# Performance work log

Hardware: AMD Instinct MI355X
Metric: run time of the kernel (lower is better)

The kernel has to match this reference:

```python
import jax, jax.numpy as jnp
import numpy as np
from jax import lax

B, N, HC = 16, 4096, 64
EPS = 1e-5


def _fps(xyz, npoint):
    # xyz: [B,N,3] -> indices [B,npoint]; deterministic start at index 0
    b, n, _ = xyz.shape
    def step(carry, _):
        dist, far = carry
        centroid = jnp.take_along_axis(xyz, far[:, None, None], axis=1)  # [B,1,3]
        d = jnp.sum((xyz - centroid) ** 2, -1)                           # [B,N]
        dist = jnp.minimum(dist, d)
        nxt = jnp.argmax(dist, -1).astype(jnp.int32)
        return (dist, nxt), far
    init = (jnp.full((b, n), 1e10, xyz.dtype), jnp.zeros((b,), jnp.int32))
    _, idx = lax.scan(step, init, None, length=npoint)
    return idx.T


def _index_points(pts, idx):
    # pts [B,N,C], idx [B,...] int -> [B,...,C]
    b = idx.shape[0]
    flat = jnp.take_along_axis(pts, idx.reshape(b, -1)[..., None], axis=1)
    return flat.reshape(idx.shape + (pts.shape[-1],))


def _ball_query(radius, nsample, xyz, new_xyz):
    # torch square_distance: ||a||^2 + ||b||^2 - 2 a.b
    n = xyz.shape[1]
    sqr = (jnp.sum(new_xyz ** 2, -1)[:, :, None] + jnp.sum(xyz ** 2, -1)[:, None, :]
           - 2.0 * jnp.einsum('bsd,bnd->bsn', new_xyz, xyz))          # [B,S,N]
    gi = jnp.where(sqr > radius ** 2, n, jnp.arange(n, dtype=jnp.int32))
    gi = jnp.sort(gi, axis=-1)[:, :, :nsample]
    first = gi[:, :, :1]
    return jnp.where(gi == n, first, gi)


def _mlp_maxpool(x, params):
    # x: [B,S,K,C]; 1x1 conv == per-point matmul; BN in training mode (batch stats)
    for (w, bb, g, be) in params:
        x = jnp.einsum('bskc,cd->bskd', x, w) + bb
        m = jnp.mean(x, axis=(0, 1, 2))
        v = jnp.var(x, axis=(0, 1, 2))
        x = g * (x - m) * lax.rsqrt(v + EPS) + be
        x = jax.nn.relu(x)
    return jnp.max(x, axis=2)  # [B,S,Cout]


def _sa(xyz, points, npoint, radius, nsample, params, group_all):
    # xyz [B,3,N], points [B,D,N] (channel-first, like torch)
    xyzt = jnp.transpose(xyz, (0, 2, 1))
    ptst = jnp.transpose(points, (0, 2, 1))
    if group_all:
        new_xyz = jnp.zeros((xyzt.shape[0], 1, 3), xyzt.dtype)
        new_pts = jnp.concatenate([xyzt[:, None], ptst[:, None]], -1)  # [B,1,N,3+D]
    else:
        fidx = _fps(xyzt, npoint)
        new_xyz = _index_points(xyzt, fidx)                            # [B,S,3]
        gi = _ball_query(radius, nsample, xyzt, new_xyz)               # [B,S,K]
        gxyz = _index_points(xyzt, gi) - new_xyz[:, :, None]           # [B,S,K,3]
        new_pts = jnp.concatenate([gxyz, _index_points(ptst, gi)], -1)
    feat = _mlp_maxpool(new_pts, params)                               # [B,S,Cout]
    return jnp.transpose(new_xyz, (0, 2, 1)), jnp.transpose(feat, (0, 2, 1))


def setup_inputs() -> dict:
    key = jax.random.key(0)
    ks = jax.random.split(key, 8)
    inp = {
        'l0_xyz': jax.random.normal(ks[0], (B, 3, N), jnp.float32),
        'l0_points': jax.random.normal(ks[1], (B, 3, N), jnp.float32),
    }
    dims = {'sa1': [(6, HC), (HC, HC * 2)],
            'sa2': [(HC * 2 + 3, HC * 2), (HC * 2, HC * 4)],
            'sa3': [(HC * 4 + 3, HC * 4), (HC * 4, HC * 8)]}
    i = 2
    for name, layers in dims.items():
        for j, (cin, cout) in enumerate(layers, 1):
            inp[f'{name}_w{j}'] = jax.random.normal(ks[i], (cin, cout), jnp.float32) * (1.0 / np.sqrt(cin))
            inp[f'{name}_b{j}'] = jnp.zeros((cout,), jnp.float32)
            inp[f'{name}_g{j}'] = jnp.ones((cout,), jnp.float32)
            inp[f'{name}_be{j}'] = jnp.zeros((cout,), jnp.float32)
            i += 1
    return inp


def reference(l0_xyz, l0_points,
              sa1_w1, sa1_b1, sa1_g1, sa1_be1, sa1_w2, sa1_b2, sa1_g2, sa1_be2,
              sa2_w1, sa2_b1, sa2_g1, sa2_be1, sa2_w2, sa2_b2, sa2_g2, sa2_be2,
              sa3_w1, sa3_b1, sa3_g1, sa3_be1, sa3_w2, sa3_b2, sa3_g2, sa3_be2):
    p1 = [(sa1_w1, sa1_b1, sa1_g1, sa1_be1), (sa1_w2, sa1_b2, sa1_g2, sa1_be2)]
    p2 = [(sa2_w1, sa2_b1, sa2_g1, sa2_be1), (sa2_w2, sa2_b2, sa2_g2, sa2_be2)]
    p3 = [(sa3_w1, sa3_b1, sa3_g1, sa3_be1), (sa3_w2, sa3_b2, sa3_g2, sa3_be2)]
    l1_xyz, l1_points = _sa(l0_xyz, l0_points, 256, 0.2, 32, p1, False)
    l2_xyz, l2_points = _sa(l1_xyz, l1_points, 128, 0.25, 64, p2, False)
    l3_xyz, l3_points = _sa(l2_xyz, l2_points, None, None, None, p3, True)
    x = l3_points.reshape(-1, HC * 8)
    return (l1_xyz, l1_points, l2_xyz, l2_points, l3_xyz, x)
```

## Files before the change

### kernel.cpp

```cpp
#include <hip/hip_runtime.h>
#include <cstddef>


#define EPSB 1e-5f
constexpr int SLOTS1 = 16;
constexpr int SLOTS2 = 64;

static __device__ __forceinline__ unsigned long long umax64(unsigned long long a,
                                                            unsigned long long b)
{
    return a > b ? a : b;
}

static __device__ __forceinline__ unsigned pack_bf16x2(float a, float b)
{
    unsigned ua = __float_as_uint(a), ub = __float_as_uint(b);
    ua += 0x7fffu + ((ua >> 16) & 1u);
    ub += 0x7fffu + ((ub >> 16) & 1u);
    return (ua >> 16) | (ub & 0xffff0000u);
}

static __device__ __forceinline__ unsigned short bf16_of(float a)
{
    unsigned u = __float_as_uint(a);
    u += 0x7fffu + ((u >> 16) & 1u);
    return (unsigned short)(u >> 16);
}

static __device__ __forceinline__ unsigned long long wave_umax64_dpp(unsigned long long x)
{
#define DPP_STEP(ctrl, rmask)                                                        \
    {                                                                                \
        int lo_ = __builtin_amdgcn_update_dpp(0, (int)(unsigned)x, ctrl, rmask, 0xf, false); \
        int hi_ = __builtin_amdgcn_update_dpp(0, (int)(unsigned)(x >> 32), ctrl, rmask, 0xf, false); \
        unsigned long long c_ = ((unsigned long long)(unsigned)hi_ << 32) | (unsigned)lo_; \
        x = umax64(x, c_);                                                           \
    }
    DPP_STEP(0x111, 0xf)
    DPP_STEP(0x112, 0xf)
    DPP_STEP(0x114, 0xf)
    DPP_STEP(0x118, 0xf)
    DPP_STEP(0x142, 0xa)
    DPP_STEP(0x143, 0xc)
#undef DPP_STEP
    unsigned lo = (unsigned)__builtin_amdgcn_readlane((int)(unsigned)x, 63);
    unsigned hi = (unsigned)__builtin_amdgcn_readlane((int)(unsigned)(x >> 32), 63);
    return ((unsigned long long)hi << 32) | lo;
}

template<int N, int NPOINT, int THREADS>
__device__ __forceinline__ void fps_body(
        unsigned long long* kslots, float4* cslots,
        const float* __restrict__ xyz, int bStride, int cStride, int nStride,
        int b, float* __restrict__ nxyz, float* __restrict__ lxyz)
{
    constexpr int PT = N / THREADS;
    constexpr int NW = THREADS / 64;
    constexpr int NSTASH = (NPOINT + THREADS - 1) / THREADS;
    const int t = threadIdx.x;
    const float* xb = xyz + (size_t)b * bStride;

    float px[PT], py[PT], pz[PT], dist[PT];
#pragma unroll
    for (int i = 0; i < PT; ++i) {
        int p = t + i * THREADS;
        px[i] = xb[(size_t)0 * cStride + (size_t)p * nStride];
        py[i] = xb[(size_t)1 * cStride + (size_t)p * nStride];
        pz[i] = xb[(size_t)2 * cStride + (size_t)p * nStride];
        dist[i] = 1e10f;
    }
    float stx[NSTASH], sty[NSTASH], stz[NSTASH];
#pragma unroll
    for (int i = 0; i < NSTASH; ++i) { stx[i] = 0.f; sty[i] = 0.f; stz[i] = 0.f; }

    float cx = xb[0], cy = xb[(size_t)cStride], cz = xb[(size_t)2 * cStride];
    if (t == 0) { stx[0] = cx; sty[0] = cy; stz[0] = cz; }

    for (int it = 1; it < NPOINT; ++it) {
        float bv = -1.0f; int bidx = 0; float bx = 0.f, by = 0.f, bz = 0.f;
#pragma unroll
        for (int i = 0; i < PT; ++i) {
            float dx = px[i] - cx, dy = py[i] - cy, dz = pz[i] - cz;
            float d = __builtin_fmaf(dx, dx, __builtin_fmaf(dy, dy, dz * dz));
            float nd = fminf(dist[i], d);
            dist[i] = nd;
            bool g = nd > bv;
            bv = g ? nd : bv;
            bidx = g ? (t + i * THREADS) : bidx;
            bx = g ? px[i] : bx; by = g ? py[i] : by; bz = g ? pz[i] : bz;
        }
        unsigned long long mykey =
            ((unsigned long long)__float_as_uint(bv) << 32) | (unsigned)(~bidx);
        unsigned long long wkey = wave_umax64_dpp(mykey);
        float wx, wy, wz;
        if constexpr (NW > 1) {
            const int pb = it & 1;
            if (mykey == wkey) {
                kslots[pb * NW + (t >> 6)] = wkey;
                cslots[pb * NW + (t >> 6)] = make_float4(bx, by, bz, 0.f);
            }
            __syncthreads();
            unsigned long long k[NW]; float4 cc[NW];
#pragma unroll
            for (int w = 0; w < NW; ++w) { k[w] = kslots[pb * NW + w]; cc[w] = cslots[pb * NW + w]; }
#pragma unroll
            for (int stp = 1; stp < NW; stp <<= 1)
#pragma unroll
                for (int w = 0; w < NW; w += 2 * stp)
                    if (k[w + stp] > k[w]) { k[w] = k[w + stp]; cc[w] = cc[w + stp]; }
            wkey = k[0]; wx = cc[0].x; wy = cc[0].y; wz = cc[0].z;
        } else {
            unsigned long long ball = __ballot(mykey == wkey);
            int wl = __ffsll(ball) - 1;
            wx = __int_as_float(__builtin_amdgcn_readlane(__float_as_int(bx), wl));
            wy = __int_as_float(__builtin_amdgcn_readlane(__float_as_int(by), wl));
            wz = __int_as_float(__builtin_amdgcn_readlane(__float_as_int(bz), wl));
        }
        if constexpr (NSTASH == 1) {
            if (t == it) { stx[0] = wx; sty[0] = wy; stz[0] = wz; }
        } else {
            if ((it & (THREADS - 1)) == t) {
                if (it >= THREADS) { stx[1] = wx; sty[1] = wy; stz[1] = wz; }
                else               { stx[0] = wx; sty[0] = wy; stz[0] = wz; }
            }
        }
        cx = wx; cy = wy; cz = wz;
    }
#pragma unroll
    for (int s2 = 0; s2 < NSTASH; ++s2) {
        int s = t + s2 * THREADS;
        if (s < NPOINT) {
            nxyz[(size_t)(b * NPOINT + s) * 3 + 0] = stx[s2];
            nxyz[(size_t)(b * NPOINT + s) * 3 + 1] = sty[s2];
            nxyz[(size_t)(b * NPOINT + s) * 3 + 2] = stz[s2];
            lxyz[(size_t)b * 3 * NPOINT + 0 * NPOINT + s] = stx[s2];
            lxyz[(size_t)b * 3 * NPOINT + 1 * NPOINT + s] = sty[s2];
            lxyz[(size_t)b * 3 * NPOINT + 2 * NPOINT + s] = stz[s2];
        }
    }
}

__global__ __launch_bounds__(512, 2)
void mega1_kernel(const float* __restrict__ l0_xyz, const float* __restrict__ l0_pts,
                  const float* __restrict__ w11, const float* __restrict__ b11,
                  float* __restrict__ p1,
                  float* __restrict__ nxyz1, float* __restrict__ o_l1xyz,
                  const float* __restrict__ w12, unsigned short* __restrict__ w12t,
                  const float* __restrict__ w22, unsigned short* __restrict__ w22t,
                  const float* __restrict__ w32, unsigned short* __restrict__ w32t,
                  float* __restrict__ stats)
{
    __shared__ unsigned long long kxs[16];
    __shared__ float4 cxs[16];
    int blk = blockIdx.x;
    const int tid = threadIdx.x;
    if (blk < 16) {
        fps_body<4096, 256, 512>(kxs, cxs, l0_xyz, 3 * 4096, 4096, 1, blk, nxyz1, o_l1xyz);
        return;
    }
    blk -= 16;
    if (blk < 8192) {
        int idx = blk * 512 + tid;
        int d = idx & 63;
        int n = (idx >> 6) & 4095;
        int b = idx >> 18;
        const float* xb = l0_xyz + (size_t)b * 3 * 4096 + n;
        const float* pb = l0_pts + (size_t)b * 3 * 4096 + n;
        float a0 = xb[0], a1 = xb[4096], a2 = xb[2 * 4096];
        float a3 = pb[0], a4 = pb[4096], a5 = pb[2 * 4096];
        float acc = b11[d];
        acc += a0 * w11[d] + a1 * w11[64 + d] + a2 * w11[128 + d];
        acc += a3 * w11[192 + d] + a4 * w11[256 + d] + a5 * w11[320 + d];
        p1[idx] = acc;
        return;
    }
    blk -= 8192;
    if (blk < 16) {
        int i = blk * 512 + tid;
        if (i < 64 * 128) { int k = i / 128, n = i % 128; w12t[(size_t)n * 64 + k] = bf16_of(w12[i]); }
        return;
    }
    blk -= 16;
    if (blk < 64) {
        int i = blk * 512 + tid;
        if (i < 128 * 256) { int k = i / 256, n = i % 256; w22t[(size_t)n * 128 + k] = bf16_of(w22[i]); }
        return;
    }
    blk -= 64;
    if (blk < 256) {
        int i = blk * 512 + tid;
        if (i < 256 * 512) { int k = i / 512, n = i % 512; w32t[(size_t)n * 256 + k] = bf16_of(w32[i]); }
        return;
    }
    blk -= 256;
    {
        int i = blk * 512 + tid;
        if (i < 129024) stats[i] = 0.f;
    }
}

template<int NS, int D, bool WITHFPS>
__global__ __launch_bounds__(64, 4)
void ballstat_kernel(const float* __restrict__ xyz, int bStride, int cStride, int nStride, int N,
                     const float* __restrict__ nxyz, int S, float r2,
                     int* __restrict__ gi,
                     const float* __restrict__ W, float* __restrict__ q,
                     const float* __restrict__ p, float* __restrict__ slots,
                     const float* __restrict__ fxyz, float* __restrict__ fnxyz,
                     float* __restrict__ flxyz)
{
    if constexpr (WITHFPS) {
        if (blockIdx.x < 16) {
            fps_body<256, 128, 64>(nullptr, nullptr, fxyz, 768, 1, 3, blockIdx.x, fnxyz, flxyz);
            return;
        }
    }
    constexpr int DL = D / 64;
    __shared__ int sgo[NS];
    int bs = blockIdx.x - (WITHFPS ? 16 : 0);
    int b = bs / S;
    int l = threadIdx.x;
    float cx = nxyz[(size_t)bs * 3 + 0], cy = nxyz[(size_t)bs * 3 + 1], cz = nxyz[(size_t)bs * 3 + 2];
    float s2 = cx * cx + cy * cy + cz * cz;
    const float* xb = xyz + (size_t)b * bStride;
    int cnt = 0;
    int first = N - 1;
    int* go = gi + (size_t)bs * NS;
    for (int base = 0; base < N; base += 64) {
        int n = base + l;
        float x = xb[(size_t)0 * cStride + (size_t)n * nStride];
        float y = xb[(size_t)1 * cStride + (size_t)n * nStride];
        float z = xb[(size_t)2 * cStride + (size_t)n * nStride];
        float x2 = x * x + y * y + z * z;
        float dot = cx * x + cy * y + cz * z;
        float sqr = (s2 + x2) - 2.0f * dot;
        bool pass = (sqr <= r2);
        unsigned long long m = __ballot(pass);
        if (cnt == 0 && m) first = base + (__ffsll((unsigned long long)m) - 1);
        int pos = cnt + __popcll(m & ((1ull << l) - 1ull));
        if (pass && pos < NS) { go[pos] = n; sgo[pos] = n; }
        cnt += __popcll(m);
        if (cnt >= NS) break;
    }
    if (cnt < NS && l >= cnt && l < NS) { go[l] = first; sgo[l] = first; }

    float qv[DL];
#pragma unroll
    for (int j = 0; j < DL; ++j) {
        int d = j * 64 + l;
        qv[j] = cx * W[d] + cy * W[D + d] + cz * W[2 * D + d];
        q[(size_t)bs * D + d] = qv[j];
    }
    float s[DL], ss[DL];
#pragma unroll
    for (int j = 0; j < DL; ++j) { s[j] = 0.f; ss[j] = 0.f; }
    for (int k = 0; k < NS; ++k) {
        int idx = sgo[k];
        const float* pr = p + (size_t)(b * N + idx) * D;
#pragma unroll
        for (int j = 0; j < DL; ++j) {
            float v = pr[j * 64 + l] - qv[j];
            s[j] += v; ss[j] += v * v;
        }
    }
    int slot = bs & (SLOTS1 - 1);
#pragma unroll
    for (int j = 0; j < DL; ++j) {
        int d = j * 64 + l;
        atomicAdd(&slots[(size_t)(slot * 2 + 0) * D + d], s[j]);
        atomicAdd(&slots[(size_t)(slot * 2 + 1) * D + d], ss[j]);
    }
}

template<int KS, int CIN, int COUTB>
__global__ __launch_bounds__(512, 2)
void mfma_gemm_kernel(const float* __restrict__ p, const float* __restrict__ q,
                      const int* __restrict__ gi, int S, int NCH, int N,
                      const float* __restrict__ st1, float m1cnt,
                      const float* __restrict__ g1, const float* __restrict__ be1,
                      const unsigned short* __restrict__ w2t, int coutFull,
                      const float* __restrict__ b2,
                      float* __restrict__ st2,
                      float* __restrict__ mx, float* __restrict__ mn)
{
    constexpr int MT = KS / 16;
    constexpr int NSL = 8 / MT;
    constexpr int SLW = COUTB / NSL;
    constexpr int TPW = SLW / 16;
    constexpr int KST = CIN / 32;
    constexpr int LDA = CIN + 8;
    typedef __attribute__((ext_vector_type(8))) short bf16x8;
    typedef __attribute__((ext_vector_type(4))) float f32x4;

    __shared__ __attribute__((aligned(16))) unsigned short hl[KS][LDA];
    __shared__ float red[4][8][SLW];
    __shared__ __attribute__((aligned(16))) float ss_scale[CIN];
    __shared__ __attribute__((aligned(16))) float ss_shift[CIN];

    const int chunk = blockIdx.x % NCH;
    const int bs = blockIdx.x / NCH;
    const int b = bs / S;
    const int tid = threadIdx.x;
    const int c2_0 = chunk * COUTB;
    const int w = tid >> 6, lane = tid & 63;
    const int mt = w % MT, ns = w / MT;
    const int lrow = lane & 15, quad = lane >> 4;

    for (int c = tid; c < CIN; c += 512) {
        float s0 = 0.f, s1 = 0.f;
        for (int sl = 0; sl < SLOTS1; ++sl) {
            s0 += st1[(size_t)(sl * 2 + 0) * CIN + c];
            s1 += st1[(size_t)(sl * 2 + 1) * CIN + c];
        }
        float mean = s0 / m1cnt;
        float var = s1 / m1cnt - mean * mean;
        float inv = 1.0f / sqrtf(var + EPSB);
        float scl = g1[c] * inv;
        ss_scale[c] = scl;
        ss_shift[c] = be1[c] - scl * mean;
    }
    __syncthreads();

    constexpr int ITER = KS * CIN / (512 * 4);
    const int gbase = bs * KS;
#pragma unroll
    for (int it = 0; it < ITER; ++it) {
        int e = (it * 512 + tid) * 4;
        int k = e / CIN, c = e % CIN;
        int row = gi ? (b * N + gi[gbase + k]) : (b * KS + k);
        float4 v = *(const float4*)&p[(size_t)row * CIN + c];
        if (q) {
            float4 qq = *(const float4*)&q[(size_t)bs * CIN + c];
            v.x -= qq.x; v.y -= qq.y; v.z -= qq.z; v.w -= qq.w;
        }
        float4 sc = *(const float4*)&ss_scale[c];
        float4 sh = *(const float4*)&ss_shift[c];
        v.x = fmaxf(__builtin_fmaf(sc.x, v.x, sh.x), 0.f);
        v.y = fmaxf(__builtin_fmaf(sc.y, v.y, sh.y), 0.f);
        v.z = fmaxf(__builtin_fmaf(sc.z, v.z, sh.z), 0.f);
        v.w = fmaxf(__builtin_fmaf(sc.w, v.w, sh.w), 0.f);
        uint2 pk;
        pk.x = pack_bf16x2(v.x, v.y);
        pk.y = pack_bf16x2(v.z, v.w);
        *(uint2*)&hl[k][c] = pk;
    }
    __syncthreads();

    f32x4 acc[TPW];
#pragma unroll
    for (int t = 0; t < TPW; ++t) acc[t] = (f32x4){0.f, 0.f, 0.f, 0.f};

    const int nbase = c2_0 + ns * SLW + lrow;
#pragma unroll
    for (int ks = 0; ks < KST; ++ks) {
        bf16x8 a = *(const bf16x8*)&hl[mt * 16 + lrow][ks * 32 + quad * 8];
#pragma unroll
        for (int t = 0; t < TPW; ++t) {
            bf16x8 bfr = *(const bf16x8*)&w2t[(size_t)(nbase + t * 16) * CIN + ks * 32 + quad * 8];
            acc[t] = __builtin_amdgcn_mfma_f32_16x16x32_bf16(a, bfr, acc[t], 0, 0, 0);
        }
    }

#pragma unroll
    for (int t = 0; t < TPW; ++t) {
        float bias = b2[nbase + t * 16];
        float s = 0.f, sq = 0.f, amx = -3.4e38f, amn = 3.4e38f;
#pragma unroll
        for (int r = 0; r < 4; ++r) {
            float v = acc[t][r] + bias;
            s += v; sq += v * v;
            amx = fmaxf(amx, v); amn = fminf(amn, v);
        }
#pragma unroll
        for (int off = 16; off < 64; off <<= 1) {
            s += __shfl_xor(s, off);
            sq += __shfl_xor(sq, off);
            amx = fmaxf(amx, __shfl_xor(amx, off));
            amn = fminf(amn, __shfl_xor(amn, off));
        }
        if (quad == 0) {
            int lc = t * 16 + lrow;
            red[0][w][lc] = s; red[1][w][lc] = sq;
            red[2][w][lc] = amx; red[3][w][lc] = amn;
        }
    }
    __syncthreads();
    for (int c = tid; c < COUTB; c += 512) {
        int ns2 = c / SLW, lc = c % SLW;
        float s = 0.f, sq = 0.f, amx = -3.4e38f, amn = 3.4e38f;
#pragma unroll
        for (int m2 = 0; m2 < MT; ++m2) {
            int w2 = ns2 * MT + m2;
            s += red[0][w2][lc]; sq += red[1][w2][lc];
            amx = fmaxf(amx, red[2][w2][lc]);
            amn = fminf(amn, red[3][w2][lc]);
        }
        int slot = blockIdx.x & (SLOTS2 - 1);
        atomicAdd(&st2[(size_t)(slot * 2 + 0) * coutFull + c2_0 + c], s);
        atomicAdd(&st2[(size_t)(slot * 2 + 1) * coutFull + c2_0 + c], sq);
        mx[(size_t)bs * coutFull + c2_0 + c] = amx;
        mn[(size_t)bs * coutFull + c2_0 + c] = amn;
    }
}

__device__ __forceinline__ void apply_body(char* smraw, int blk, int nblk,
        const float* __restrict__ st2, int C, float cnt,
        const float* __restrict__ g2, const float* __restrict__ be2,
        const float* __restrict__ mx, const float* __restrict__ mn,
        int S, float* __restrict__ outT, int total, float* __restrict__ zero48)
{
    float* sc = (float*)smraw;
    float* sh = sc + 512;
    for (int c = threadIdx.x; c < C; c += 512) {
        float s0 = 0.f, s1 = 0.f;
        for (int sl = 0; sl < SLOTS2; ++sl) {
            s0 += st2[(size_t)(sl * 2 + 0) * C + c];
            s1 += st2[(size_t)(sl * 2 + 1) * C + c];
        }
        float mean = s0 / cnt;
        float var = s1 / cnt - mean * mean;
        float inv = 1.0f / sqrtf(var + EPSB);
        float scl = g2[c] * inv;
        sc[c] = scl; sh[c] = be2[c] - scl * mean;
    }
    __syncthreads();
    if (zero48 && blk == 0 && threadIdx.x < 48) zero48[threadIdx.x] = 0.f;
    for (int e = blk * 512 + threadIdx.x; e < total; e += nblk * 512) {
        int s = e % S;
        int rem = e / S;
        int c = rem % C;
        int b = rem / C;
        float scl = sc[c];
        size_t mi = (size_t)(b * S + s) * C + c;
        float v = (scl >= 0.f) ? mx[mi] : mn[mi];
        outT[e] = fmaxf(scl * v + sh[c], 0.f);
    }
}

template<int COUTB, bool DOSTATS>
__device__ __forceinline__ void proj_body(char* smraw, int blk,
        const float* __restrict__ xyzsrc,
        const float* __restrict__ mxF, const float* __restrict__ mnF,
        const float* __restrict__ stF, const float* __restrict__ gF,
        const float* __restrict__ beF, float cntF,
        int N, int CF, const float* __restrict__ W, int coutFull,
        const float* __restrict__ bias, float* __restrict__ outp,
        float* __restrict__ st3)
{
    constexpr int BK = 32, BKP = 36, TK = 4, TC = 4, THREADS = 512, ROWS = 64;
    constexpr int C2G = COUTB / TC;
    float (*al)[BKP] = (float (*)[BKP])smraw;
    float (*wl)[BKP] = (float (*)[BKP])(smraw + ROWS * BKP * 4);
    float* scF = (float*)(smraw + (ROWS + COUTB) * BKP * 4);
    float* shF = scF + CF;
    float* red2 = shF + CF;
    const int NCH = coutFull / COUTB;
    const int chunk = blk % NCH;
    const int rb = blk / NCH;
    const int m0 = rb * ROWS;
    const int c2_0 = chunk * COUTB;
    const int K = CF + 3;
    const int tid = threadIdx.x;
    const int c2g = tid % C2G, kt = tid / C2G;

    for (int c = tid; c < CF; c += THREADS) {
        float s0 = 0.f, s1 = 0.f;
        for (int sl = 0; sl < SLOTS2; ++sl) {
            s0 += stF[(size_t)(sl * 2 + 0) * CF + c];
            s1 += stF[(size_t)(sl * 2 + 1) * CF + c];
        }
        float mean = s0 / cntF;
        float var = s1 / cntF - mean * mean;
        float inv = 1.0f / sqrtf(var + EPSB);
        float scl = gF[c] * inv;
        scF[c] = scl; shF[c] = beF[c] - scl * mean;
    }

    float acc[TK][TC];
#pragma unroll
    for (int i = 0; i < TK; ++i)
#pragma unroll
        for (int j = 0; j < TC; ++j) acc[i][j] = 0.f;
    const int npan = (K + BK - 1) / BK;
    for (int pan = 0; pan < npan; ++pan) {
        __syncthreads();
        const int cbase = pan * BK;
        for (int e = tid; e < ROWS * BK; e += THREADS) {
            int rl = e / BK, cl = e % BK;
            int c = cbase + cl;
            int m = m0 + rl;
            float v = 0.f;
            if (c < 3) v = xyzsrc[(size_t)m * 3 + c];
            else if (c < K) {
                int cf = c - 3;
                float scl = scF[cf];
                size_t mi = (size_t)m * CF + cf;
                float pick = (scl >= 0.f) ? mxF[mi] : mnF[mi];
                v = fmaxf(scl * pick + shF[cf], 0.f);
            }
            al[rl][cl] = v;
        }
        for (int e = tid; e < COUTB * BK; e += THREADS) {
            int c2 = e % COUTB, cl = e / COUTB;
            int c = cbase + cl;
            wl[c2][cl] = (c < K) ? W[(size_t)c * coutFull + c2_0 + c2] : 0.f;
        }
        __syncthreads();
#pragma unroll
        for (int cl = 0; cl < BK; cl += 4) {
            float4 av[TK], wv[TC];
#pragma unroll
            for (int i = 0; i < TK; ++i) av[i] = *(const float4*)&al[kt * TK + i][cl];
#pragma unroll
            for (int j = 0; j < TC; ++j) wv[j] = *(const float4*)&wl[c2g + j * C2G][cl];
#pragma unroll
            for (int i = 0; i < TK; ++i)
#pragma unroll
                for (int j = 0; j < TC; ++j)
                    acc[i][j] += av[i].x * wv[j].x + av[i].y * wv[j].y
                               + av[i].z * wv[j].z + av[i].w * wv[j].w;
        }
    }
    float ps[TC], pq[TC];
#pragma unroll
    for (int j = 0; j < TC; ++j) {
        float bb_ = bias[c2_0 + c2g + j * C2G];
        float s = 0.f, sq = 0.f;
#pragma unroll
        for (int i = 0; i < TK; ++i) {
            int m = m0 + kt * TK + i;
            float v = acc[i][j] + bb_;
            outp[(size_t)m * coutFull + c2_0 + c2g + j * C2G] = v;
            s += v; sq += v * v;
        }
        ps[j] = s; pq[j] = sq;
    }
    if constexpr (DOSTATS) {
        const int w = tid >> 6, lane = tid & 63;
#pragma unroll
        for (int j = 0; j < TC; ++j) {
            ps[j] += __shfl_xor(ps[j], 32);
            pq[j] += __shfl_xor(pq[j], 32);
            if (lane < 32) {
                int c2 = c2g + j * C2G;
                red2[(w * COUTB + c2) * 2 + 0] = ps[j];
                red2[(w * COUTB + c2) * 2 + 1] = pq[j];
            }
        }
        __syncthreads();
        for (int c = tid; c < COUTB; c += THREADS) {
            float s = 0.f, sq = 0.f;
#pragma unroll
            for (int w2 = 0; w2 < 8; ++w2) {
                s += red2[(w2 * COUTB + c) * 2 + 0];
                sq += red2[(w2 * COUTB + c) * 2 + 1];
            }
            int slot = blk & (SLOTS1 - 1);
            atomicAdd(&st3[(size_t)(slot * 2 + 0) * coutFull + c2_0 + c], s);
            atomicAdd(&st3[(size_t)(slot * 2 + 1) * coutFull + c2_0 + c], sq);
        }
    }
}

template<bool DOSTATS>
__global__ __launch_bounds__(512, 2)
void applyproj_kernel(
        const float* __restrict__ xyzsrc,
        const float* __restrict__ mxF, const float* __restrict__ mnF,
        const float* __restrict__ stF, const float* __restrict__ gF,
        const float* __restrict__ beF, float cntF,
        int Nrows, int CF, const float* __restrict__ W, int coutFull,
        const float* __restrict__ bias, float* __restrict__ outp,
        float* __restrict__ st3, int projBlocks,
        const float* __restrict__ st2, int C, float m2cnt,
        const float* __restrict__ g2, const float* __restrict__ be2,
        const float* __restrict__ mxA, const float* __restrict__ mnA,
        int S, float* __restrict__ outT, int total)
{
    __shared__ __attribute__((aligned(16))) char arena[38144];
    if ((int)blockIdx.x < projBlocks)
        proj_body<128, DOSTATS>(arena, blockIdx.x, xyzsrc, mxF, mnF, stF, gF, beF, cntF,
                                Nrows, CF, W, coutFull, bias, outp, st3);
    else
        apply_body(arena, blockIdx.x - projBlocks, gridDim.x - projBlocks,
                   st2, C, m2cnt, g2, be2, mxA, mnA, S, outT, total, nullptr);
}

__global__ __launch_bounds__(512, 2)
void apply3_kernel(const float* __restrict__ st2, int C, float cnt,
                   const float* __restrict__ g2, const float* __restrict__ be2,
                   const float* __restrict__ mx, const float* __restrict__ mn,
                   int S, float* __restrict__ outT, int total, float* __restrict__ zero48)
{
    __shared__ __attribute__((aligned(16))) char arena[4160];
    apply_body(arena, blockIdx.x, gridDim.x, st2, C, cnt, g2, be2, mx, mn, S, outT, total, zero48);
}

extern "C" void kernel_launch(void* const* d_in, const int* in_sizes, int n_in,
                              void* d_out, int out_size, void* d_ws, size_t ws_size,
                              hipStream_t stream)
{
    (void)in_sizes; (void)n_in; (void)out_size; (void)ws_size;
    const float* l0_xyz = (const float*)d_in[0];
    const float* l0_pts = (const float*)d_in[1];
    const float* w11 = (const float*)d_in[2];  const float* b11 = (const float*)d_in[3];
    const float* g11 = (const float*)d_in[4];  const float* be11 = (const float*)d_in[5];
    const float* w12 = (const float*)d_in[6];  const float* b12 = (const float*)d_in[7];
    const float* g12 = (const float*)d_in[8];  const float* be12 = (const float*)d_in[9];
    const float* w21 = (const float*)d_in[10]; const float* b21 = (const float*)d_in[11];
    const float* g21 = (const float*)d_in[12]; const float* be21 = (const float*)d_in[13];
    const float* w22 = (const float*)d_in[14]; const float* b22 = (const float*)d_in[15];
    const float* g22 = (const float*)d_in[16]; const float* be22 = (const float*)d_in[17];
    const float* w31 = (const float*)d_in[18]; const float* b31 = (const float*)d_in[19];
    const float* g31 = (const float*)d_in[20]; const float* be31 = (const float*)d_in[21];
    const float* w32 = (const float*)d_in[22]; const float* b32 = (const float*)d_in[23];
    const float* g32 = (const float*)d_in[24]; const float* be32 = (const float*)d_in[25];

    float* out = (float*)d_out;
    float* o_l1xyz = out;
    float* o_l1pts = out + 12288;
    float* o_l2xyz = out + 536576;
    float* o_l2pts = out + 542720;
    float* o_l3xyz = out + 1067008;
    float* o_x     = out + 1067056;

    char* ws = (char*)d_ws;
    size_t off = 0;
    auto alloc = [&](size_t bytes) {
        void* r = ws + off;
        off += ((bytes + 255) & ~(size_t)255);
        return r;
    };
    float* nxyz1 = (float*)alloc(12288 * 4);
    float* nxyz2 = (float*)alloc(6144 * 4);
    int*   gi1   = (int*)alloc(131072 * 4);
    int*   gi2   = (int*)alloc(131072 * 4);
    float* p1    = (float*)alloc(4194304 * 4);
    float* q1    = (float*)alloc(262144 * 4);
    float* mx1   = (float*)alloc(524288 * 4);
    float* mn1   = (float*)alloc(524288 * 4);
    float* p2    = (float*)alloc(524288 * 4);
    float* q2    = (float*)alloc(262144 * 4);
    float* mx2   = (float*)alloc(524288 * 4);
    float* mn2   = (float*)alloc(524288 * 4);
    float* h31   = (float*)alloc(524288 * 4);
    float* mx3   = (float*)alloc(8192 * 4);
    float* mn3   = (float*)alloc(8192 * 4);
    float* stats = (float*)alloc(129024 * 4);
    float* st1a = stats;
    float* st2a = st1a + 2048;
    float* st1b = st2a + 16384;
    float* st2b = st1b + 4096;
    float* st3a = st2b + 32768;
    float* st3b = st3a + 8192;
    unsigned short* w12t = (unsigned short*)alloc(128 * 64 * 2);
    unsigned short* w22t = (unsigned short*)alloc(256 * 128 * 2);
    unsigned short* w32t = (unsigned short*)alloc(512 * 256 * 2);

    mega1_kernel<<<8796, 512, 0, stream>>>(l0_xyz, l0_pts, w11, b11, p1,
                                           nxyz1, o_l1xyz,
                                           w12, w12t, w22, w22t, w32, w32t, stats);
    ballstat_kernel<32, 64, true><<<4112, 64, 0, stream>>>(
        l0_xyz, 3 * 4096, 4096, 1, 4096, nxyz1, 256, 0.04f, gi1, w11, q1, p1, st1a,
        nxyz1, nxyz2, o_l2xyz);
    mfma_gemm_kernel<32, 64, 128><<<4096, 512, 0, stream>>>(
        p1, q1, gi1, 256, 1, 4096, st1a, 131072.0f, g11, be11, w12t, 128, b12,
        st2a, mx1, mn1);
    applyproj_kernel<false><<<128, 512, 0, stream>>>(
        nxyz1, mx1, mn1, st2a, g12, be12, 131072.0f, 256, 128, w21, 128, b21, p2,
        nullptr, 64,
        st2a, 128, 131072.0f, g12, be12, mx1, mn1, 256, o_l1pts, 524288);
    ballstat_kernel<64, 128, false><<<2048, 64, 0, stream>>>(
        nxyz1, 768, 1, 3, 256, nxyz2, 128, 0.0625f, gi2, w21, q2, p2, st1b,
        nullptr, nullptr, nullptr);
    mfma_gemm_kernel<64, 128, 256><<<2048, 512, 0, stream>>>(
        p2, q2, gi2, 128, 1, 256, st1b, 131072.0f, g21, be21, w22t, 256, b22,
        st2b, mx2, mn2);
    applyproj_kernel<true><<<128, 512, 0, stream>>>(
        nxyz2, mx2, mn2, st2b, g22, be22, 131072.0f, 128, 256, w31, 256, b31, h31,
        st3a, 64,
        st2b, 256, 131072.0f, g22, be22, mx2, mn2, 128, o_l2pts, 524288);
    mfma_gemm_kernel<128, 256, 128><<<64, 512, 0, stream>>>(
        h31, nullptr, nullptr, 1, 4, 0, st3a, 2048.0f, g31, be31, w32t, 512, b32,
        st3b, mx3, mn3);
    apply3_kernel<<<16, 512, 0, stream>>>(st3b, 512, 2048.0f, g32, be32, mx3, mn3,
                                          1, o_x, 8192, o_l3xyz);
}
```

Baseline: 660.1 us.

## Resolve FPS winner via shared-memory coordinate lookup and pack ballstat waves

```diff
diff --git a/kernel.cpp b/kernel.cpp
--- a/kernel.cpp
+++ b/kernel.cpp
@@ -49,15 +49,14 @@
 }
 
 template<int N, int NPOINT, int THREADS>
-__device__ __forceinline__ void fps_body(
-        unsigned long long* kslots, float4* cslots,
+__device__ __forceinline__ void fps_body(int t,
+        float* sx, float* sy, float* sz, unsigned long long* kslots,
         const float* __restrict__ xyz, int bStride, int cStride, int nStride,
         int b, float* __restrict__ nxyz, float* __restrict__ lxyz)
 {
     constexpr int PT = N / THREADS;
     constexpr int NW = THREADS / 64;
     constexpr int NSTASH = (NPOINT + THREADS - 1) / THREADS;
-    const int t = threadIdx.x;
     const float* xb = xyz + (size_t)b * bStride;
 
     float px[PT], py[PT], pz[PT], dist[PT];
@@ -67,17 +66,24 @@
         px[i] = xb[(size_t)0 * cStride + (size_t)p * nStride];
         py[i] = xb[(size_t)1 * cStride + (size_t)p * nStride];
         pz[i] = xb[(size_t)2 * cStride + (size_t)p * nStride];
+        if constexpr (NW > 1) { sx[p] = px[i]; sy[p] = py[i]; sz[p] = pz[i]; }
         dist[i] = 1e10f;
     }
+#pragma unroll
+    for (int i = 0; i < PT; ++i)
+        asm volatile("" : "+v"(px[i]), "+v"(py[i]), "+v"(pz[i]));
+
     float stx[NSTASH], sty[NSTASH], stz[NSTASH];
 #pragma unroll
     for (int i = 0; i < NSTASH; ++i) { stx[i] = 0.f; sty[i] = 0.f; stz[i] = 0.f; }
 
     float cx = xb[0], cy = xb[(size_t)cStride], cz = xb[(size_t)2 * cStride];
     if (t == 0) { stx[0] = cx; sty[0] = cy; stz[0] = cz; }
+    if constexpr (NW > 1) __syncthreads();
 
     for (int it = 1; it < NPOINT; ++it) {
-        float bv = -1.0f; int bidx = 0; float bx = 0.f, by = 0.f, bz = 0.f;
+        float bv = -1.0f; int bidx = 0;
+        float bx = 0.f, by = 0.f, bz = 0.f;
 #pragma unroll
         for (int i = 0; i < PT; ++i) {
             float dx = px[i] - cx, dy = py[i] - cy, dz = pz[i] - cz;
@@ -87,44 +93,41 @@
             bool g = nd > bv;
             bv = g ? nd : bv;
             bidx = g ? (t + i * THREADS) : bidx;
-            bx = g ? px[i] : bx; by = g ? py[i] : by; bz = g ? pz[i] : bz;
+            if constexpr (NW == 1) {
+                bx = g ? px[i] : bx; by = g ? py[i] : by; bz = g ? pz[i] : bz;
+            }
         }
         unsigned long long mykey =
             ((unsigned long long)__float_as_uint(bv) << 32) | (unsigned)(~bidx);
         unsigned long long wkey = wave_umax64_dpp(mykey);
-        float wx, wy, wz;
         if constexpr (NW > 1) {
             const int pb = it & 1;
-            if (mykey == wkey) {
-                kslots[pb * NW + (t >> 6)] = wkey;
-                cslots[pb * NW + (t >> 6)] = make_float4(bx, by, bz, 0.f);
+            if ((t & 63) == 0) kslots[pb * NW + (t >> 6)] = wkey;
+            __syncthreads();
+            const ulonglong2* kp = (const ulonglong2*)(kslots + pb * NW);
+            unsigned long long m = wkey;
+#pragma unroll
+            for (int w2 = 0; w2 < NW / 2; ++w2) {
+                ulonglong2 kk = kp[w2];
+                m = umax64(m, umax64(kk.x, kk.y));
             }
-            __syncthreads();
-            unsigned long long k[NW]; float4 cc[NW];
-#pragma unroll
-            for (int w = 0; w < NW; ++w) { k[w] = kslots[pb * NW + w]; cc[w] = cslots[pb * NW + w]; }
-#pragma unroll
-            for (int stp = 1; stp < NW; stp <<= 1)
-#pragma unroll
-                for (int w = 0; w < NW; w += 2 * stp)
-                    if (k[w + stp] > k[w]) { k[w] = k[w + stp]; cc[w] = cc[w + stp]; }
-            wkey = k[0]; wx = cc[0].x; wy = cc[0].y; wz = cc[0].z;
+            int widx = (int)(~(unsigned)m);
+            cx = sx[widx]; cy = sy[widx]; cz = sz[widx];
         } else {
             unsigned long long ball = __ballot(mykey == wkey);
             int wl = __ffsll(ball) - 1;
-            wx = __int_as_float(__builtin_amdgcn_readlane(__float_as_int(bx), wl));
-            wy = __int_as_float(__builtin_amdgcn_readlane(__float_as_int(by), wl));
-            wz = __int_as_float(__builtin_amdgcn_readlane(__float_as_int(bz), wl));
+            cx = __int_as_float(__builtin_amdgcn_readlane(__float_as_int(bx), wl));
+            cy = __int_as_float(__builtin_amdgcn_readlane(__float_as_int(by), wl));
+            cz = __int_as_float(__builtin_amdgcn_readlane(__float_as_int(bz), wl));
         }
         if constexpr (NSTASH == 1) {
-            if (t == it) { stx[0] = wx; sty[0] = wy; stz[0] = wz; }
+            if (t == it) { stx[0] = cx; sty[0] = cy; stz[0] = cz; }
         } else {
             if ((it & (THREADS - 1)) == t) {
-                if (it >= THREADS) { stx[1] = wx; sty[1] = wy; stz[1] = wz; }
-                else               { stx[0] = wx; sty[0] = wy; stz[0] = wz; }
+                if (it >= THREADS) { stx[1] = cx; sty[1] = cy; stz[1] = cz; }
+                else               { stx[0] = cx; sty[0] = cy; stz[0] = cz; }
             }
         }
-        cx = wx; cy = wy; cz = wz;
     }
 #pragma unroll
     for (int s2 = 0; s2 < NSTASH; ++s2) {
@@ -140,7 +143,7 @@
     }
 }
 
-__global__ __launch_bounds__(512, 2)
+__global__ __launch_bounds__(512)
 void mega1_kernel(const float* __restrict__ l0_xyz, const float* __restrict__ l0_pts,
                   const float* __restrict__ w11, const float* __restrict__ b11,
                   float* __restrict__ p1,
@@ -150,12 +153,13 @@
                   const float* __restrict__ w32, unsigned short* __restrict__ w32t,
                   float* __restrict__ stats)
 {
-    __shared__ unsigned long long kxs[16];
-    __shared__ float4 cxs[16];
+    __shared__ float smx[4096], smy[4096], smz[4096];
+    __shared__ __attribute__((aligned(16))) unsigned long long kxs[16];
     int blk = blockIdx.x;
     const int tid = threadIdx.x;
     if (blk < 16) {
-        fps_body<4096, 256, 512>(kxs, cxs, l0_xyz, 3 * 4096, 4096, 1, blk, nxyz1, o_l1xyz);
+        fps_body<4096, 256, 512>(tid, smx, smy, smz, kxs,
+                                 l0_xyz, 3 * 4096, 4096, 1, blk, nxyz1, o_l1xyz);
         return;
     }
     blk -= 16;
@@ -200,7 +204,7 @@
 }
 
 template<int NS, int D, bool WITHFPS>
-__global__ __launch_bounds__(64, 4)
+__global__ __launch_bounds__(256)
 void ballstat_kernel(const float* __restrict__ xyz, int bStride, int cStride, int nStride, int N,
                      const float* __restrict__ nxyz, int S, float r2,
                      int* __restrict__ gi,
@@ -209,17 +213,20 @@
                      const float* __restrict__ fxyz, float* __restrict__ fnxyz,
                      float* __restrict__ flxyz)
 {
+    __shared__ int sgo[4][NS];
+    const int wid = threadIdx.x >> 6, l = threadIdx.x & 63;
+    int g = blockIdx.x * 4 + wid;
     if constexpr (WITHFPS) {
-        if (blockIdx.x < 16) {
-            fps_body<256, 128, 64>(nullptr, nullptr, fxyz, 768, 1, 3, blockIdx.x, fnxyz, flxyz);
+        if (g < 16) {
+            fps_body<256, 128, 64>(l, nullptr, nullptr, nullptr, nullptr,
+                                   fxyz, 768, 1, 3, g, fnxyz, flxyz);
             return;
         }
+        g -= 16;
     }
     constexpr int DL = D / 64;
-    __shared__ int sgo[NS];
-    int bs = blockIdx.x - (WITHFPS ? 16 : 0);
-    int b = bs / S;
-    int l = threadIdx.x;
+    const int bs = g;
+    const int b = bs / S;
     float cx = nxyz[(size_t)bs * 3 + 0], cy = nxyz[(size_t)bs * 3 + 1], cz = nxyz[(size_t)bs * 3 + 2];
     float s2 = cx * cx + cy * cy + cz * cz;
     const float* xb = xyz + (size_t)b * bStride;
@@ -238,11 +245,11 @@
         unsigned long long m = __ballot(pass);
         if (cnt == 0 && m) first = base + (__ffsll((unsigned long long)m) - 1);
         int pos = cnt + __popcll(m & ((1ull << l) - 1ull));
-        if (pass && pos < NS) { go[pos] = n; sgo[pos] = n; }
+        if (pass && pos < NS) { go[pos] = n; sgo[wid][pos] = n; }
         cnt += __popcll(m);
         if (cnt >= NS) break;
     }
-    if (cnt < NS && l >= cnt && l < NS) { go[l] = first; sgo[l] = first; }
+    if (cnt < NS && l >= cnt && l < NS) { go[l] = first; sgo[wid][l] = first; }
 
     float qv[DL];
 #pragma unroll
@@ -255,7 +262,7 @@
 #pragma unroll
     for (int j = 0; j < DL; ++j) { s[j] = 0.f; ss[j] = 0.f; }
     for (int k = 0; k < NS; ++k) {
-        int idx = sgo[k];
+        int idx = sgo[wid][k];
         const float* pr = p + (size_t)(b * N + idx) * D;
 #pragma unroll
         for (int j = 0; j < DL; ++j) {
@@ -660,7 +667,7 @@
     mega1_kernel<<<8796, 512, 0, stream>>>(l0_xyz, l0_pts, w11, b11, p1,
                                            nxyz1, o_l1xyz,
                                            w12, w12t, w22, w22t, w32, w32t, stats);
-    ballstat_kernel<32, 64, true><<<4112, 64, 0, stream>>>(
+    ballstat_kernel<32, 64, true><<<1028, 256, 0, stream>>>(
         l0_xyz, 3 * 4096, 4096, 1, 4096, nxyz1, 256, 0.04f, gi1, w11, q1, p1, st1a,
         nxyz1, nxyz2, o_l2xyz);
     mfma_gemm_kernel<32, 64, 128><<<4096, 512, 0, stream>>>(
@@ -670,7 +677,7 @@
         nxyz1, mx1, mn1, st2a, g12, be12, 131072.0f, 256, 128, w21, 128, b21, p2,
         nullptr, 64,
         st2a, 128, 131072.0f, g12, be12, mx1, mn1, 256, o_l1pts, 524288);
-    ballstat_kernel<64, 128, false><<<2048, 64, 0, stream>>>(
+    ballstat_kernel<64, 128, false><<<512, 256, 0, stream>>>(
         nxyz1, 768, 1, 3, 256, nxyz2, 128, 0.0625f, gi2, w21, q2, p2, st1b,
         nullptr, nullptr, nullptr);
     mfma_gemm_kernel<64, 128, 256><<<2048, 512, 0, stream>>>(
```

Result: faster. 528.5 us (-19.9%).
